# Kernel optimization log

Measured on AMD Instinct MI355X. Metric: run time of the kernel, lower is better.

## Reference

```python
import jax, jax.numpy as jnp
import numpy as np

NUM_HEADS = 128
QK_NOPE = 128
QK_ROPE = 64
V_HEAD = 128
Q_HEAD_DIM = 192
SOFTMAX_SCALE = 1.0 / np.sqrt(192.0)


def _rope_interleave(x, cos, sin):
    # x: [b,h,s,d]; reorder interleaved pairs to half-split layout then rotate
    b, h, s, d = x.shape
    x = x.reshape(b, h, s, d // 2, 2).swapaxes(3, 4).reshape(b, h, s, d)
    x1, x2 = x[..., : d // 2], x[..., d // 2:]
    rot = jnp.concatenate([-x2, x1], axis=-1)
    return x * cos + rot * sin


def setup_inputs() -> dict:
    key = jax.random.key(0)
    ks = jax.random.split(key, 8)
    bsz, q_len = 16, 1
    q_lora, kv_lora = 1536, 512
    cache_cap = 4096
    start_pos = 2048
    s = 0.05
    q_normed_dn = jax.random.normal(ks[0], (bsz, q_len, q_lora), jnp.float32) * s
    compressed_kv = jax.random.normal(ks[1], (bsz, q_len, kv_lora), jnp.float32) * s
    k_pe = jax.random.normal(ks[2], (bsz, 1, q_len, QK_ROPE), jnp.float32) * s
    position_ids = jnp.full((bsz, q_len), start_pos, dtype=jnp.int64)
    ckv_cache = jax.random.normal(ks[3], (bsz, cache_cap, kv_lora), jnp.float32) * s
    k_pe_cache = jax.random.normal(ks[4], (bsz, cache_cap, QK_ROPE), jnp.float32) * s
    # rope caches over full positions
    pos = jnp.arange(cache_cap, dtype=jnp.float32)
    inv = 1.0 / (10000.0 ** (jnp.arange(0, QK_ROPE, 2, dtype=jnp.float32) / QK_ROPE))
    freqs = pos[:, None] * inv[None, :]
    emb = jnp.concatenate([freqs, freqs], axis=-1)
    sin_cache = jnp.sin(emb)
    cos_cache = jnp.cos(emb)
    wkv_b = jax.random.normal(ks[5], (NUM_HEADS, QK_NOPE + V_HEAD, kv_lora), jnp.float32) * s
    wq_b = jax.random.normal(ks[6], (NUM_HEADS * Q_HEAD_DIM, q_lora), jnp.float32) * s
    return {
        "q_normed_dn": q_normed_dn,
        "compressed_kv": compressed_kv,
        "k_pe": k_pe,
        "position_ids": position_ids,
        "start_pos": start_pos,
        "ckv_cache": ckv_cache,
        "k_pe_cache": k_pe_cache,
        "sin_cache": sin_cache,
        "cos_cache": cos_cache,
        "wkv_b": wkv_b,
        "wq_b": wq_b,
    }


def reference(q_normed_dn, compressed_kv, k_pe, position_ids, start_pos,
              ckv_cache, k_pe_cache, sin_cache, cos_cache, wkv_b, wq_b):
    bsz, q_len, q_lora = q_normed_dn.shape
    kv_lora = compressed_kv.shape[-1]

    # split absorbed query projection
    wq_b_t = wq_b.T.reshape(q_lora, NUM_HEADS, Q_HEAD_DIM)  # [l,h,192]
    q_nope = jnp.einsum('bsl,lhd->bhsd', q_normed_dn, wq_b_t[:, :, :QK_NOPE])
    q_pe = jnp.einsum('bsl,lhd->bhsd', q_normed_dn, wq_b_t[:, :, QK_NOPE:])

    # matrix absorption: q_nope projected into latent space via w_ukv
    w_ukv = wkv_b[:, :QK_NOPE]                         # [h,128,c]
    q_nope = jnp.einsum('bshd,hdc->bshc', q_nope.swapaxes(1, 2), w_ukv)  # [b,s,h,c]

    # RoPE on q_pe and k_pe using gathered cos/sin at position_ids
    cos = cos_cache[position_ids][:, None]   # [b,1,s,d]
    sin = sin_cache[position_ids][:, None]
    q_pe = _rope_interleave(q_pe, cos, sin)            # [b,h,s,64]
    k_pe = _rope_interleave(k_pe, cos, sin)            # [b,1,s,64]
    q_pe = q_pe.swapaxes(1, 2)                         # [b,s,h,64]
    k_pe = k_pe[:, 0]                                  # [b,s,64]

    # append new tokens to caches at start_pos (q_len new tokens)
    ckv_cache = jax.lax.dynamic_update_slice(ckv_cache, compressed_kv, (0, start_pos, 0))
    k_pe_cache = jax.lax.dynamic_update_slice(k_pe_cache, k_pe, (0, start_pos, 0))
    kv_len = start_pos + q_len
    ckv = ckv_cache[:, :kv_len]                        # [b,n,c]
    kpe = k_pe_cache[:, :kv_len]                       # [b,n,64]

    # MLA decode attention in latent space (q_len==1, causal trivially satisfied)
    # scores = q_nope . ckv + q_pe . kpe
    scores = (jnp.einsum('bshc,bnc->bhsn', q_nope, ckv) +
              jnp.einsum('bshd,bnd->bhsn', q_pe, kpe)) * SOFTMAX_SCALE
    probs = jax.nn.softmax(scores, axis=-1)
    o = jnp.einsum('bhsn,bnc->bshc', probs, ckv)       # [b,s,h,c]
    o = o.reshape(bsz * q_len, NUM_HEADS, kv_lora)

    # project latent output to v_head_dim via tail of wkv_b
    attn_output = jnp.einsum('bhc,hdc->bhd', o, wkv_b[:, -V_HEAD:])
    return attn_output
```

## Files before the change

kernel.cpp:

```cpp
#include <hip/hip_runtime.h>
#include <hip/hip_bf16.h>
#include <math.h>

typedef __attribute__((ext_vector_type(8))) short short8x;
typedef __attribute__((ext_vector_type(4))) float f32x4;
typedef __attribute__((ext_vector_type(4))) unsigned short u16x4;
typedef __attribute__((ext_vector_type(8))) unsigned short u16x8;

#define NSPLIT 16
#define NTILE 66
#define KVROWS (NTILE * 32)

__device__ __forceinline__ unsigned short f2bf(float x) {
  unsigned int u = __float_as_uint(x);
  u += 0x7fffu + ((u >> 16) & 1u);
  return (unsigned short)(u >> 16);
}
__device__ __forceinline__ float bf2f(unsigned short u) {
  return __uint_as_float(((unsigned int)u) << 16);
}
__device__ __forceinline__ u16x4 cvt4(float4 v) {
  u16x4 r;
  r[0] = f2bf(v.x); r[1] = f2bf(v.y); r[2] = f2bf(v.z); r[3] = f2bf(v.w);
  return r;
}
__device__ __forceinline__ void gload_lds16(const void* g, void* l) {
  __builtin_amdgcn_global_load_lds(
      (const __attribute__((address_space(1))) unsigned int*)g,
      (__attribute__((address_space(3))) unsigned int*)l, 16, 0, 0);
}

__global__ __launch_bounds__(256) void kP_prep(
    const float* __restrict__ ckvc, const float* __restrict__ kpec,
    const float* __restrict__ ckvn, const float* __restrict__ kpein,
    const float* __restrict__ cosc, const float* __restrict__ sinc,
    const int* __restrict__ sposp, int cap,
    unsigned short* __restrict__ kvbf,
    const float* __restrict__ x,
    unsigned short* __restrict__ xh, unsigned short* __restrict__ xl) {
  const int bx = blockIdx.x;
  const int tid = threadIdx.x;
  const int spos = sposp[0];

  if (bx < 2376) {
#pragma unroll
    for (int i = 0; i < 8; ++i) {
      const int u = bx * 2048 + i * 256 + tid;
      const int b = u / 304128;
      const int r = u - b * 304128;
      const int n = r / 144;
      const int c4 = (r - n * 144) * 4;
      float4 v = make_float4(0.f, 0.f, 0.f, 0.f);
      if (n < spos) {
        if (c4 < 512) v = *(const float4*)(ckvc + ((size_t)b * cap + n) * 512 + c4);
        else          v = *(const float4*)(kpec + ((size_t)b * cap + n) * 64 + (c4 - 512));
      } else if (n == spos) {
        if (c4 < 512) v = *(const float4*)(ckvn + (size_t)b * 512 + c4);
        else {
          const int d = c4 - 512;
          const float* kp = kpein + b * 64;
          float o[4];
          if (d < 32) {
#pragma unroll
            for (int k = 0; k < 4; ++k) {
              int j = d + k;
              o[k] = kp[2 * j] * cosc[spos * 64 + j] - kp[2 * j + 1] * sinc[spos * 64 + j];
            }
          } else {
#pragma unroll
            for (int k = 0; k < 4; ++k) {
              int j = d - 32 + k;
              o[k] = kp[2 * j + 1] * cosc[spos * 64 + j] + kp[2 * j] * sinc[spos * 64 + j];
            }
          }
          v = make_float4(o[0], o[1], o[2], o[3]);
        }
      }
      *(u16x4*)(kvbf + (size_t)u * 4) = cvt4(v);
    }
  } else {
#pragma unroll
    for (int i = 0; i < 24; ++i) {
      const int u = i * 256 + tid;
      const float4 v = *(const float4*)(x + u * 4);
      const float vf[4] = {v.x, v.y, v.z, v.w};
      u16x4 h, l;
#pragma unroll
      for (int k = 0; k < 4; ++k) {
        const unsigned int uu = __float_as_uint(vf[k]);
        const unsigned int hb = uu & 0xffff0000u;
        h[k] = (unsigned short)(hb >> 16);
        l[k] = f2bf(vf[k] - __uint_as_float(hb));
      }
      *(u16x4*)(xh + u * 4) = h;
      *(u16x4*)(xl + u * 4) = l;
    }
  }
}

__global__ __launch_bounds__(256) void kVT(
    const unsigned short* __restrict__ kvbf, unsigned short* __restrict__ vT) {
  __shared__ __align__(16) unsigned short tile_sh[32 * 576];
  const int v_ = blockIdx.x;
  const int b = v_ / NTILE;
  const int tile = v_ - b * NTILE;
  const int tid = threadIdx.x;
  const int wid = tid >> 6;
  const unsigned short* src = kvbf + ((size_t)b * KVROWS + tile * 32) * 576;

#pragma unroll
  for (int i = 0; i < 9; ++i) {
    const int ch = i * 256 + tid;
    const int row = ch / 72, cc = ch - row * 72;
    gload_lds16(src + row * 576 + ((cc ^ (row & 7)) * 8),
                &tile_sh[(i * 256 + wid * 64) * 8]);
  }
  __syncthreads();

  unsigned short* vdst = vT + ((size_t)b * NTILE + tile) * 18432;
#pragma unroll
  for (int r = 0; r < 9; ++r) {
    const int c = r * 64 + (tid >> 2);
    const int q = tid & 3;
    const int c8 = c >> 3, c7 = c & 7;
    u16x8 w;
#pragma unroll
    for (int j = 0; j < 8; ++j)
      w[j] = tile_sh[(q * 8 + j) * 576 + ((c8 ^ j) << 3) + c7];
    *(u16x8*)(vdst + c * 32 + q * 8) = w;
  }
}

__global__ __launch_bounds__(256) void k1q(
    const float* __restrict__ wq,
    const unsigned short* __restrict__ xh, const unsigned short* __restrict__ xl,
    float* __restrict__ qfull) {
  const int tid = threadIdx.x;
  const int lane = tid & 63, wid = tid >> 6;
  const int l15 = lane & 15, lg = lane >> 4;
  const int rowb = blockIdx.x * 64 + wid * 16;
  const float* wrow = wq + (size_t)(rowb + l15) * 1536 + lg * 8;
  const unsigned short* xhp = xh + l15 * 1536 + lg * 8;
  const unsigned short* xlp = xl + l15 * 1536 + lg * 8;

  f32x4 acc = (f32x4){0.f, 0.f, 0.f, 0.f};
#pragma unroll 8
  for (int kc = 0; kc < 48; ++kc) {
    const float4 wA = *(const float4*)(wrow + kc * 32);
    const float4 wB = *(const float4*)(wrow + kc * 32 + 4);
    const short8x bh = *(const short8x*)(xhp + kc * 32);
    const short8x bl = *(const short8x*)(xlp + kc * 32);
    const float wf[8] = {wA.x, wA.y, wA.z, wA.w, wB.x, wB.y, wB.z, wB.w};
    short8x ah, al;
#pragma unroll
    for (int e = 0; e < 8; ++e) {
      const unsigned int uu = __float_as_uint(wf[e]);
      const unsigned int hb = uu & 0xffff0000u;
      ah[e] = (short)(hb >> 16);
      al[e] = (short)f2bf(wf[e] - __uint_as_float(hb));
    }
    acc = __builtin_amdgcn_mfma_f32_16x16x32_bf16(ah, bh, acc, 0, 0, 0);
    acc = __builtin_amdgcn_mfma_f32_16x16x32_bf16(ah, bl, acc, 0, 0, 0);
    acc = __builtin_amdgcn_mfma_f32_16x16x32_bf16(al, bh, acc, 0, 0, 0);
  }
#pragma unroll
  for (int r = 0; r < 4; ++r)
    qfull[(size_t)l15 * 24576 + rowb + lg * 4 + r] = acc[r];
}

__global__ __launch_bounds__(256) void kB_q(
    const float* __restrict__ qfull, const float* __restrict__ wkv,
    const float* __restrict__ cosc, const float* __restrict__ sinc,
    const int* __restrict__ sposp, unsigned short* __restrict__ qcat) {
  __shared__ float qs[16 * 128];
  const int bx = blockIdx.x;
  const int tid = threadIdx.x;
  if (bx < 256) {
    const int h = bx & 127;
    const int half = bx >> 7;
    for (int u = tid; u < 2048; u += 256) {
      int bb = u >> 7, d = u & 127;
      qs[u] = qfull[bb * 24576 + h * 192 + d];
    }
    __syncthreads();
    const int c = half * 256 + tid;
    float acc[16];
#pragma unroll
    for (int bb = 0; bb < 16; ++bb) acc[bb] = 0.f;
    const float* wbase = wkv + (size_t)h * 256 * 512;
    for (int d = 0; d < 128; ++d) {
      const float w = wbase[d * 512 + c];
#pragma unroll
      for (int bb = 0; bb < 16; ++bb) acc[bb] += qs[bb * 128 + d] * w;
    }
#pragma unroll
    for (int bb = 0; bb < 16; ++bb)
      qcat[(size_t)(bb * 128 + h) * 576 + c] = f2bf(acc[bb]);
  } else {
    const int b = bx - 256;
    const int pos = sposp[0];
#pragma unroll
    for (int i = 0; i < 16; ++i) {
      int idx = tid + i * 256;
      int h = idx >> 5, j = idx & 31;
      const float cj = cosc[pos * 64 + j];
      const float sj = sinc[pos * 64 + j];
      const float* src = qfull + b * 24576 + h * 192 + 128;
      float x0 = src[2 * j], x1 = src[2 * j + 1];
      unsigned short* dst = qcat + (size_t)(b * 128 + h) * 576 + 512;
      dst[j] = f2bf(x0 * cj - x1 * sj);
      dst[j + 32] = f2bf(x1 * cj + x0 * sj);
    }
  }
}

__global__ __launch_bounds__(512, 2) void k4_attn(
    const unsigned short* __restrict__ kvbf, const unsigned short* __restrict__ vT,
    const unsigned short* __restrict__ qcat, const int* __restrict__ sposp,
    unsigned short* __restrict__ opart, float* __restrict__ mlp) {
  __shared__ __align__(16) unsigned short kv_sh[2][32 * 576];
  __shared__ __align__(16) unsigned short vt_sh[2][512 * 32];
  __shared__ __align__(16) unsigned short p_sh[8 * 640];

  const int tid = threadIdx.x;
  const int split = blockIdx.x, b = blockIdx.y;
  const int kvlen = sposp[0] + 1;
  const int lane = tid & 63, wid = tid >> 6;
  const int l15 = lane & 15, lg = lane >> 4;

  const unsigned short* kvb = kvbf + (size_t)b * KVROWS * 576;
  const unsigned short* vtb = vT + (size_t)b * NTILE * 18432;

  auto STAGE = [&](int pb, int tt) {
    const unsigned short* ksrc = kvb + (size_t)tt * 32 * 576;
    for (int j = wid; j < 36; j += 8) {
      int u = j * 64 + lane;
      int row = u / 72, cc = u - row * 72;
      gload_lds16(ksrc + row * 576 + ((cc ^ (row & 7)) * 8), &kv_sh[pb][j * 512]);
    }
    const unsigned short* vsrc = vtb + (size_t)tt * 18432;
    for (int j = wid; j < 32; j += 8)
      gload_lds16(vsrc + j * 512 + lane * 8, &vt_sh[pb][j * 512]);
  };

  STAGE(0, split);

  const int hrow = b * 128 + wid * 16 + l15;
  const unsigned short* qrow = qcat + (size_t)hrow * 576;
  short8x qf[18];
#pragma unroll
  for (int s = 0; s < 18; ++s)
    qf[s] = *(const short8x*)(qrow + s * 32 + lg * 8);

  f32x4 acc[32];
#pragma unroll
  for (int i = 0; i < 32; ++i) acc[i] = (f32x4){0.f, 0.f, 0.f, 0.f};
  float mold[4] = {-1e30f, -1e30f, -1e30f, -1e30f};
  float lsum[4] = {0.f, 0.f, 0.f, 0.f};
  const float C2 = (1.0f / sqrtf(192.0f)) * 1.4426950408889634f;

  int pb = 0;
  for (int tt = split; tt * 32 < kvlen; tt += NSPLIT, pb ^= 1) {
    __syncthreads();
    if ((tt + NSPLIT) * 32 < kvlen) STAGE(pb ^ 1, tt + NSPLIT);
    const int n0 = tt * 32;

    f32x4 D0 = (f32x4){0.f, 0.f, 0.f, 0.f};
    f32x4 D1 = (f32x4){0.f, 0.f, 0.f, 0.f};
#pragma unroll
    for (int s = 0; s < 18; ++s) {
      const int c8 = (s * 4 + lg) ^ (l15 & 7);
      short8x fb0 = *(const short8x*)&kv_sh[pb][l15 * 576 + c8 * 8];
      short8x fb1 = *(const short8x*)&kv_sh[pb][(16 + l15) * 576 + c8 * 8];
      D0 = __builtin_amdgcn_mfma_f32_16x16x32_bf16(qf[s], fb0, D0, 0, 0, 0);
      D1 = __builtin_amdgcn_mfma_f32_16x16x32_bf16(qf[s], fb1, D1, 0, 0, 0);
    }

    const bool v0 = (n0 + l15) < kvlen;
    const bool v1 = (n0 + 16 + l15) < kvlen;
    float alpha[4];
#pragma unroll
    for (int r = 0; r < 4; ++r) {
      const float t0 = v0 ? D0[r] * C2 : -1e30f;
      const float t1 = v1 ? D1[r] * C2 : -1e30f;
      float mx = fmaxf(t0, t1);
      mx = fmaxf(mx, __shfl_xor(mx, 1, 64));
      mx = fmaxf(mx, __shfl_xor(mx, 2, 64));
      mx = fmaxf(mx, __shfl_xor(mx, 4, 64));
      mx = fmaxf(mx, __shfl_xor(mx, 8, 64));
      const float mn = fmaxf(mold[r], mx);
      alpha[r] = exp2f(mold[r] - mn);
      const float p0 = v0 ? exp2f(t0 - mn) : 0.f;
      const float p1 = v1 ? exp2f(t1 - mn) : 0.f;
      float rs = p0 + p1;
      rs += __shfl_xor(rs, 1, 64);
      rs += __shfl_xor(rs, 2, 64);
      rs += __shfl_xor(rs, 4, 64);
      rs += __shfl_xor(rs, 8, 64);
      lsum[r] = lsum[r] * alpha[r] + rs;
      mold[r] = mn;
      p_sh[wid * 640 + (lg * 4 + r) * 40 + l15] = f2bf(p0);
      p_sh[wid * 640 + (lg * 4 + r) * 40 + 16 + l15] = f2bf(p1);
    }
    const f32x4 av = {alpha[0], alpha[1], alpha[2], alpha[3]};
#pragma unroll
    for (int cg = 0; cg < 32; ++cg) acc[cg] *= av;

    const short8x pa = *(const short8x*)&p_sh[wid * 640 + l15 * 40 + lg * 8];
#pragma unroll
    for (int cg = 0; cg < 32; ++cg) {
      short8x bv = *(const short8x*)&vt_sh[pb][cg * 512 + l15 * 32 + lg * 8];
      acc[cg] = __builtin_amdgcn_mfma_f32_16x16x32_bf16(pa, bv, acc[cg], 0, 0, 0);
    }
  }

  const int hbm_ = b * 128 + wid * 16 + lg * 4;
  if (l15 == 0) {
#pragma unroll
    for (int r = 0; r < 4; ++r) {
      mlp[(size_t)(hbm_ + r) * (2 * NSPLIT) + split * 2] = mold[r];
      mlp[(size_t)(hbm_ + r) * (2 * NSPLIT) + split * 2 + 1] = lsum[r];
    }
  }

  __syncthreads();
  unsigned short* ep = &kv_sh[0][0] + wid * 8192;
#pragma unroll
  for (int cg = 0; cg < 32; ++cg)
#pragma unroll
    for (int r = 0; r < 4; ++r)
      ep[(lg * 4 + r) * 512 + cg * 16 + l15] = f2bf(acc[cg][r]);
#pragma unroll
  for (int r16 = 0; r16 < 16; ++r16) {
    const int bh = b * 128 + wid * 16 + r16;
    const size_t ob = ((size_t)bh * NSPLIT + split) * 512;
#pragma unroll
    for (int i = 0; i < 2; ++i)
      *(u16x4*)&opart[ob + i * 256 + lane * 4] =
          *(const u16x4*)&ep[r16 * 512 + i * 256 + lane * 4];
  }
}

__global__ __launch_bounds__(512) void kC_out(
    const unsigned short* __restrict__ opart, const float* __restrict__ mlp,
    const float* __restrict__ wkv, float* __restrict__ out) {
  __shared__ float os[16 * 512];
  __shared__ float wsc[16 * 16];
  __shared__ float lsc[16];
  const int h = blockIdx.x;
  const int tid = threadIdx.x;

  if (tid < 16) {
    const int b = tid;
    const float* m = mlp + (size_t)(b * 128 + h) * (2 * NSPLIT);
    float mi[NSPLIT], li[NSPLIT], M = -1e30f;
#pragma unroll
    for (int i = 0; i < NSPLIT; ++i) {
      mi[i] = m[i * 2];
      li[i] = m[i * 2 + 1];
      M = fmaxf(M, mi[i]);
    }
    float Ls = 0.f;
#pragma unroll
    for (int i = 0; i < NSPLIT; ++i) {
      const float w = exp2f(mi[i] - M);
      Ls += li[i] * w;
      wsc[b * NSPLIT + i] = w;
    }
    lsc[b] = Ls;
  }
  __syncthreads();

  for (int u = tid; u < 8192; u += 512) {
    const int b = u >> 9, c = u & 511;
    const unsigned short* op = opart + (size_t)(b * 128 + h) * NSPLIT * 512 + c;
    float o = 0.f;
#pragma unroll
    for (int i = 0; i < NSPLIT; ++i) o += wsc[b * NSPLIT + i] * bf2f(op[i * 512]);
    os[u] = o / lsc[b];
  }
  __syncthreads();

  const int d = tid >> 2, cq = tid & 3;
  const float* wrow = wkv + ((size_t)(h * 256 + 128 + d)) * 512;
  float acc[16];
#pragma unroll
  for (int bb = 0; bb < 16; ++bb) acc[bb] = 0.f;
  for (int i = 0; i < 32; ++i) {
    const int c = cq * 4 + i * 16;
    const float4 w4 = *(const float4*)&wrow[c];
#pragma unroll
    for (int bb = 0; bb < 16; ++bb) {
      const float4 o4 = *(const float4*)&os[bb * 512 + c];
      acc[bb] += w4.x * o4.x + w4.y * o4.y + w4.z * o4.z + w4.w * o4.w;
    }
  }
#pragma unroll
  for (int bb = 0; bb < 16; ++bb) {
    float v = acc[bb];
    v += __shfl_xor(v, 1, 64);
    v += __shfl_xor(v, 2, 64);
    if (cq == 0) out[(size_t)(bb * 128 + h) * 128 + d] = v;
  }
}

extern "C" void kernel_launch(void* const* d_in, const int* in_sizes, int n_in,
                              void* d_out, int out_size, void* d_ws, size_t ws_size,
                              hipStream_t stream) {
  const float* x = (const float*)d_in[0];
  const float* ckvn = (const float*)d_in[1];
  const float* kpein = (const float*)d_in[2];
  const int* sposp = (const int*)d_in[4];
  const float* ckvc = (const float*)d_in[5];
  const float* kpec = (const float*)d_in[6];
  const float* sinc = (const float*)d_in[7];
  const float* cosc = (const float*)d_in[8];
  const float* wkv = (const float*)d_in[9];
  const float* wq = (const float*)d_in[10];
  float* out = (float*)d_out;

  const int cap = in_sizes[5] / (16 * 512);

  float* ws = (float*)d_ws;
  float* qfull = ws;
  float* mlp = ws + 393216;
  unsigned short* qcat = (unsigned short*)(ws + 458752);
  unsigned short* xh   = (unsigned short*)(ws + 1048576);
  unsigned short* xl   = (unsigned short*)(ws + 1060864);
  unsigned short* kvbf = (unsigned short*)(ws + 1073152);
  unsigned short* vT   = (unsigned short*)(ws + 10805248);
  unsigned short* opart = (unsigned short*)(ws + 20537344);

  kP_prep<<<dim3(2377), 256, 0, stream>>>(ckvc, kpec, ckvn, kpein, cosc, sinc,
                                          sposp, cap, kvbf, x, xh, xl);
  kVT<<<dim3(1056), 256, 0, stream>>>(kvbf, vT);
  k1q<<<dim3(384), 256, 0, stream>>>(wq, xh, xl, qfull);
  kB_q<<<dim3(272), 256, 0, stream>>>(qfull, wkv, cosc, sinc, sposp, qcat);
  k4_attn<<<dim3(NSPLIT, 16), 512, 0, stream>>>(kvbf, vT, qcat, sposp, opart, mlp);
  kC_out<<<dim3(128), 512, 0, stream>>>(opart, mlp, wkv, out);
}
```

Measured before the change: 184.9 us.

## Fuse KV bf16 conversion with V transpose and split x in GEMM

Merges the KV-cache bf16 conversion kernel and the separate V-transpose kernel into one per-tile kernel. It loads fp32 rows into LDS with a swizzle and writes both the row-major bf16 K copy and the transposed V copy, so the bf16 intermediate is no longer re-read. The hi/lo bf16 split of the query input moves into the q-projection GEMM, removing the xh/xl buffers and one launch. The cost is that fp32 is read twice: once from global memory for K and once via LDS for V. The LDS tile also doubles to 72KB, which may lower occupancy.

```diff
diff --git a/kernel.cpp b/kernel.cpp
--- a/kernel.cpp
+++ b/kernel.cpp
@@ -30,26 +30,75 @@
       (__attribute__((address_space(3))) unsigned int*)l, 16, 0, 0);
 }
 
-__global__ __launch_bounds__(256) void kP_prep(
+__global__ __launch_bounds__(256) void kPV(
     const float* __restrict__ ckvc, const float* __restrict__ kpec,
     const float* __restrict__ ckvn, const float* __restrict__ kpein,
     const float* __restrict__ cosc, const float* __restrict__ sinc,
     const int* __restrict__ sposp, int cap,
-    unsigned short* __restrict__ kvbf,
-    const float* __restrict__ x,
-    unsigned short* __restrict__ xh, unsigned short* __restrict__ xl) {
-  const int bx = blockIdx.x;
+    unsigned short* __restrict__ kvbf, unsigned short* __restrict__ vT) {
+  __shared__ __align__(16) float tile_sh[32 * 576];
+  const int v_ = blockIdx.x;
+  const int b = v_ / NTILE;
+  const int tile = v_ - b * NTILE;
+  const int n0 = tile * 32;
   const int tid = threadIdx.x;
+  const int wid = tid >> 6;
   const int spos = sposp[0];
 
-  if (bx < 2376) {
-#pragma unroll
-    for (int i = 0; i < 8; ++i) {
-      const int u = bx * 2048 + i * 256 + tid;
-      const int b = u / 304128;
-      const int r = u - b * 304128;
-      const int n = r / 144;
-      const int c4 = (r - n * 144) * 4;
+  unsigned short* kdst = kvbf + ((size_t)b * KVROWS + n0) * 576;
+  unsigned short* vdst = vT + ((size_t)b * NTILE + tile) * 18432;
+
+  if (n0 + 31 < spos) {
+    const float* cbase = ckvc + ((size_t)b * cap + n0) * 512;
+    const float* pbase = kpec + ((size_t)b * cap + n0) * 64;
+#pragma unroll
+    for (int i = 0; i < 18; ++i) {
+      const int ch = i * 256 + tid;
+      const int row = ch / 144, cc = ch - row * 144;
+      const int gc = cc ^ (row & 7);
+      const float* src = (gc < 128) ? cbase + (size_t)row * 512 + gc * 4
+                                    : pbase + (size_t)row * 64 + (gc - 128) * 4;
+      gload_lds16(src, &tile_sh[(i * 256 + wid * 64) * 4]);
+    }
+#pragma unroll
+    for (int i = 0; i < 9; ++i) {
+      const int oc = i * 256 + tid;
+      const int row = oc / 72, p = oc - row * 72;
+      const int c0 = p * 8;
+      float4 a, c2;
+      if (c0 < 512) {
+        a  = *(const float4*)(cbase + (size_t)row * 512 + c0);
+        c2 = *(const float4*)(cbase + (size_t)row * 512 + c0 + 4);
+      } else {
+        a  = *(const float4*)(pbase + (size_t)row * 64 + (c0 - 512));
+        c2 = *(const float4*)(pbase + (size_t)row * 64 + (c0 - 512) + 4);
+      }
+      const u16x4 wa = cvt4(a), wb = cvt4(c2);
+      u16x8 w;
+#pragma unroll
+      for (int k = 0; k < 4; ++k) { w[k] = wa[k]; w[4 + k] = wb[k]; }
+      *(u16x8*)(kdst + row * 576 + c0) = w;
+    }
+    __syncthreads();
+#pragma unroll
+    for (int r = 0; r < 9; ++r) {
+      const int c = r * 64 + (tid >> 2);
+      const int q = tid & 3;
+      const int gc = c >> 2, c3 = c & 3;
+      u16x8 w;
+#pragma unroll
+      for (int j = 0; j < 8; ++j) {
+        const int n = q * 8 + j;
+        w[j] = f2bf(tile_sh[n * 576 + ((gc ^ j) << 2) + c3]);
+      }
+      *(u16x8*)(vdst + c * 32 + q * 8) = w;
+    }
+  } else if (n0 <= spos) {
+#pragma unroll
+    for (int i = 0; i < 18; ++i) {
+      const int u = i * 256 + tid;
+      const int row = u / 144, c4 = (u - row * 144) * 4;
+      const int n = n0 + row;
       float4 v = make_float4(0.f, 0.f, 0.f, 0.f);
       if (n < spos) {
         if (c4 < 512) v = *(const float4*)(ckvc + ((size_t)b * cap + n) * 512 + c4);
@@ -76,88 +125,77 @@
           v = make_float4(o[0], o[1], o[2], o[3]);
         }
       }
-      *(u16x4*)(kvbf + (size_t)u * 4) = cvt4(v);
+      *(u16x4*)(kdst + row * 576 + c4) = cvt4(v);
+    }
+#pragma unroll
+    for (int i = 0; i < 18; ++i) {
+      const int o = i * 256 + tid;
+      const int c = o >> 3;
+      const int n4 = (o & 7) * 4;
+      u16x4 w;
+#pragma unroll
+      for (int k = 0; k < 4; ++k) {
+        const int n = n0 + n4 + k;
+        float x = 0.f;
+        if (n < spos) {
+          x = (c < 512) ? ckvc[((size_t)b * cap + n) * 512 + c]
+                        : kpec[((size_t)b * cap + n) * 64 + (c - 512)];
+        } else if (n == spos) {
+          if (c < 512) x = ckvn[(size_t)b * 512 + c];
+          else {
+            const int d = c - 512;
+            const float* kp = kpein + b * 64;
+            const int j = (d < 32) ? d : d - 32;
+            const float cj = cosc[spos * 64 + j], sj = sinc[spos * 64 + j];
+            x = (d < 32) ? kp[2 * j] * cj - kp[2 * j + 1] * sj
+                         : kp[2 * j + 1] * cj + kp[2 * j] * sj;
+          }
+        }
+        w[k] = f2bf(x);
+      }
+      *(u16x4*)(vdst + c * 32 + n4) = w;
     }
   } else {
-#pragma unroll
-    for (int i = 0; i < 24; ++i) {
-      const int u = i * 256 + tid;
-      const float4 v = *(const float4*)(x + u * 4);
-      const float vf[4] = {v.x, v.y, v.z, v.w};
-      u16x4 h, l;
-#pragma unroll
-      for (int k = 0; k < 4; ++k) {
-        const unsigned int uu = __float_as_uint(vf[k]);
-        const unsigned int hb = uu & 0xffff0000u;
-        h[k] = (unsigned short)(hb >> 16);
-        l[k] = f2bf(vf[k] - __uint_as_float(hb));
-      }
-      *(u16x4*)(xh + u * 4) = h;
-      *(u16x4*)(xl + u * 4) = l;
-    }
-  }
-}
-
-__global__ __launch_bounds__(256) void kVT(
-    const unsigned short* __restrict__ kvbf, unsigned short* __restrict__ vT) {
-  __shared__ __align__(16) unsigned short tile_sh[32 * 576];
-  const int v_ = blockIdx.x;
-  const int b = v_ / NTILE;
-  const int tile = v_ - b * NTILE;
-  const int tid = threadIdx.x;
-  const int wid = tid >> 6;
-  const unsigned short* src = kvbf + ((size_t)b * KVROWS + tile * 32) * 576;
-
-#pragma unroll
-  for (int i = 0; i < 9; ++i) {
-    const int ch = i * 256 + tid;
-    const int row = ch / 72, cc = ch - row * 72;
-    gload_lds16(src + row * 576 + ((cc ^ (row & 7)) * 8),
-                &tile_sh[(i * 256 + wid * 64) * 8]);
-  }
-  __syncthreads();
-
-  unsigned short* vdst = vT + ((size_t)b * NTILE + tile) * 18432;
-#pragma unroll
-  for (int r = 0; r < 9; ++r) {
-    const int c = r * 64 + (tid >> 2);
-    const int q = tid & 3;
-    const int c8 = c >> 3, c7 = c & 7;
-    u16x8 w;
-#pragma unroll
-    for (int j = 0; j < 8; ++j)
-      w[j] = tile_sh[(q * 8 + j) * 576 + ((c8 ^ j) << 3) + c7];
-    *(u16x8*)(vdst + c * 32 + q * 8) = w;
+    const u16x8 z = {0, 0, 0, 0, 0, 0, 0, 0};
+#pragma unroll
+    for (int i = 0; i < 9; ++i) {
+      const int oc = i * 256 + tid;
+      *(u16x8*)(kdst + oc * 8) = z;
+      *(u16x8*)(vdst + oc * 8) = z;
+    }
   }
 }
 
 __global__ __launch_bounds__(256) void k1q(
-    const float* __restrict__ wq,
-    const unsigned short* __restrict__ xh, const unsigned short* __restrict__ xl,
+    const float* __restrict__ wq, const float* __restrict__ x,
     float* __restrict__ qfull) {
   const int tid = threadIdx.x;
   const int lane = tid & 63, wid = tid >> 6;
   const int l15 = lane & 15, lg = lane >> 4;
   const int rowb = blockIdx.x * 64 + wid * 16;
   const float* wrow = wq + (size_t)(rowb + l15) * 1536 + lg * 8;
-  const unsigned short* xhp = xh + l15 * 1536 + lg * 8;
-  const unsigned short* xlp = xl + l15 * 1536 + lg * 8;
+  const float* xrow = x + l15 * 1536 + lg * 8;
 
   f32x4 acc = (f32x4){0.f, 0.f, 0.f, 0.f};
 #pragma unroll 8
   for (int kc = 0; kc < 48; ++kc) {
     const float4 wA = *(const float4*)(wrow + kc * 32);
     const float4 wB = *(const float4*)(wrow + kc * 32 + 4);
-    const short8x bh = *(const short8x*)(xhp + kc * 32);
-    const short8x bl = *(const short8x*)(xlp + kc * 32);
+    const float4 xA = *(const float4*)(xrow + kc * 32);
+    const float4 xB = *(const float4*)(xrow + kc * 32 + 4);
     const float wf[8] = {wA.x, wA.y, wA.z, wA.w, wB.x, wB.y, wB.z, wB.w};
-    short8x ah, al;
+    const float xf[8] = {xA.x, xA.y, xA.z, xA.w, xB.x, xB.y, xB.z, xB.w};
+    short8x ah, al, bh, bl;
 #pragma unroll
     for (int e = 0; e < 8; ++e) {
-      const unsigned int uu = __float_as_uint(wf[e]);
-      const unsigned int hb = uu & 0xffff0000u;
+      unsigned int uu = __float_as_uint(wf[e]);
+      unsigned int hb = uu & 0xffff0000u;
       ah[e] = (short)(hb >> 16);
       al[e] = (short)f2bf(wf[e] - __uint_as_float(hb));
+      uu = __float_as_uint(xf[e]);
+      hb = uu & 0xffff0000u;
+      bh[e] = (short)(hb >> 16);
+      bl[e] = (short)f2bf(xf[e] - __uint_as_float(hb));
     }
     acc = __builtin_amdgcn_mfma_f32_16x16x32_bf16(ah, bh, acc, 0, 0, 0);
     acc = __builtin_amdgcn_mfma_f32_16x16x32_bf16(ah, bl, acc, 0, 0, 0);
@@ -425,16 +463,13 @@
   float* qfull = ws;
   float* mlp = ws + 393216;
   unsigned short* qcat = (unsigned short*)(ws + 458752);
-  unsigned short* xh   = (unsigned short*)(ws + 1048576);
-  unsigned short* xl   = (unsigned short*)(ws + 1060864);
-  unsigned short* kvbf = (unsigned short*)(ws + 1073152);
-  unsigned short* vT   = (unsigned short*)(ws + 10805248);
-  unsigned short* opart = (unsigned short*)(ws + 20537344);
-
-  kP_prep<<<dim3(2377), 256, 0, stream>>>(ckvc, kpec, ckvn, kpein, cosc, sinc,
-                                          sposp, cap, kvbf, x, xh, xl);
-  kVT<<<dim3(1056), 256, 0, stream>>>(kvbf, vT);
-  k1q<<<dim3(384), 256, 0, stream>>>(wq, xh, xl, qfull);
+  unsigned short* kvbf = (unsigned short*)(ws + 1048576);
+  unsigned short* vT   = (unsigned short*)(ws + 10780672);
+  unsigned short* opart = (unsigned short*)(ws + 20512768);
+
+  kPV<<<dim3(NTILE * 16), 256, 0, stream>>>(ckvc, kpec, ckvn, kpein, cosc, sinc,
+                                            sposp, cap, kvbf, vT);
+  k1q<<<dim3(384), 256, 0, stream>>>(wq, x, qfull);
   kB_q<<<dim3(272), 256, 0, stream>>>(qfull, wkv, cosc, sinc, sposp, qcat);
   k4_attn<<<dim3(NSPLIT, 16), 512, 0, stream>>>(kvbf, vT, qcat, sposp, opart, mlp);
   kC_out<<<dim3(128), 512, 0, stream>>>(opart, mlp, wkv, out);
```

Measured after the change: 202.4 us. 9.4% more time.

## Merge prep, q-projection and V-transpose kernels into fewer launches; swizzle V LDS

Applied to the files above, without the earlier changes.

Fuses the fp32 q projection (now splitting x into hi/lo bf16 inline, so the separate xh/xl pass goes away) into the KV bf16 conversion kernel as extra blocks. The V-transpose kernel is folded into the q-absorption kernel as extra blocks, cutting six launches to four and letting independent work share the GPU. The attention kernel also applies an XOR swizzle to the V tile layout in LDS to reduce bank conflicts on the P·V reads. The cost is repeated hi/lo conversion of x in every q block and a larger shared allocation for the merged kernel.

```diff
diff --git a/kernel.cpp b/kernel.cpp
--- a/kernel.cpp
+++ b/kernel.cpp
@@ -30,22 +30,58 @@
       (__attribute__((address_space(3))) unsigned int*)l, 16, 0, 0);
 }
 
-__global__ __launch_bounds__(256) void kP_prep(
+__global__ __launch_bounds__(256) void kA(
     const float* __restrict__ ckvc, const float* __restrict__ kpec,
     const float* __restrict__ ckvn, const float* __restrict__ kpein,
     const float* __restrict__ cosc, const float* __restrict__ sinc,
     const int* __restrict__ sposp, int cap,
     unsigned short* __restrict__ kvbf,
-    const float* __restrict__ x,
-    unsigned short* __restrict__ xh, unsigned short* __restrict__ xl) {
+    const float* __restrict__ wq, const float* __restrict__ x,
+    float* __restrict__ qfull) {
   const int bx = blockIdx.x;
   const int tid = threadIdx.x;
-  const int spos = sposp[0];
-
-  if (bx < 2376) {
+
+  if (bx < 384) {
+    const int lane = tid & 63, wid = tid >> 6;
+    const int l15 = lane & 15, lg = lane >> 4;
+    const int rowb = bx * 64 + wid * 16;
+    const float* wrow = wq + (size_t)(rowb + l15) * 1536 + lg * 8;
+    const float* xrow = x + l15 * 1536 + lg * 8;
+
+    f32x4 acc = (f32x4){0.f, 0.f, 0.f, 0.f};
+#pragma unroll 8
+    for (int kc = 0; kc < 48; ++kc) {
+      const float4 wA = *(const float4*)(wrow + kc * 32);
+      const float4 wB = *(const float4*)(wrow + kc * 32 + 4);
+      const float4 xA = *(const float4*)(xrow + kc * 32);
+      const float4 xB = *(const float4*)(xrow + kc * 32 + 4);
+      const float wf[8] = {wA.x, wA.y, wA.z, wA.w, wB.x, wB.y, wB.z, wB.w};
+      const float xf[8] = {xA.x, xA.y, xA.z, xA.w, xB.x, xB.y, xB.z, xB.w};
+      short8x ah, al, bh, bl;
+#pragma unroll
+      for (int e = 0; e < 8; ++e) {
+        unsigned int uu = __float_as_uint(wf[e]);
+        unsigned int hb = uu & 0xffff0000u;
+        ah[e] = (short)(hb >> 16);
+        al[e] = (short)f2bf(wf[e] - __uint_as_float(hb));
+        uu = __float_as_uint(xf[e]);
+        hb = uu & 0xffff0000u;
+        bh[e] = (short)(hb >> 16);
+        bl[e] = (short)f2bf(xf[e] - __uint_as_float(hb));
+      }
+      acc = __builtin_amdgcn_mfma_f32_16x16x32_bf16(ah, bh, acc, 0, 0, 0);
+      acc = __builtin_amdgcn_mfma_f32_16x16x32_bf16(ah, bl, acc, 0, 0, 0);
+      acc = __builtin_amdgcn_mfma_f32_16x16x32_bf16(al, bh, acc, 0, 0, 0);
+    }
+#pragma unroll
+    for (int r = 0; r < 4; ++r)
+      qfull[(size_t)l15 * 24576 + rowb + lg * 4 + r] = acc[r];
+  } else {
+    const int bxx = bx - 384;
+    const int spos = sposp[0];
 #pragma unroll
     for (int i = 0; i < 8; ++i) {
-      const int u = bx * 2048 + i * 256 + tid;
+      const int u = bxx * 2048 + i * 256 + tid;
       const int b = u / 304128;
       const int r = u - b * 304128;
       const int n = r / 144;
@@ -78,104 +114,20 @@
       }
       *(u16x4*)(kvbf + (size_t)u * 4) = cvt4(v);
     }
-  } else {
-#pragma unroll
-    for (int i = 0; i < 24; ++i) {
-      const int u = i * 256 + tid;
-      const float4 v = *(const float4*)(x + u * 4);
-      const float vf[4] = {v.x, v.y, v.z, v.w};
-      u16x4 h, l;
-#pragma unroll
-      for (int k = 0; k < 4; ++k) {
-        const unsigned int uu = __float_as_uint(vf[k]);
-        const unsigned int hb = uu & 0xffff0000u;
-        h[k] = (unsigned short)(hb >> 16);
-        l[k] = f2bf(vf[k] - __uint_as_float(hb));
-      }
-      *(u16x4*)(xh + u * 4) = h;
-      *(u16x4*)(xl + u * 4) = l;
-    }
-  }
-}
-
-__global__ __launch_bounds__(256) void kVT(
-    const unsigned short* __restrict__ kvbf, unsigned short* __restrict__ vT) {
-  __shared__ __align__(16) unsigned short tile_sh[32 * 576];
-  const int v_ = blockIdx.x;
-  const int b = v_ / NTILE;
-  const int tile = v_ - b * NTILE;
-  const int tid = threadIdx.x;
-  const int wid = tid >> 6;
-  const unsigned short* src = kvbf + ((size_t)b * KVROWS + tile * 32) * 576;
-
-#pragma unroll
-  for (int i = 0; i < 9; ++i) {
-    const int ch = i * 256 + tid;
-    const int row = ch / 72, cc = ch - row * 72;
-    gload_lds16(src + row * 576 + ((cc ^ (row & 7)) * 8),
-                &tile_sh[(i * 256 + wid * 64) * 8]);
-  }
-  __syncthreads();
-
-  unsigned short* vdst = vT + ((size_t)b * NTILE + tile) * 18432;
-#pragma unroll
-  for (int r = 0; r < 9; ++r) {
-    const int c = r * 64 + (tid >> 2);
-    const int q = tid & 3;
-    const int c8 = c >> 3, c7 = c & 7;
-    u16x8 w;
-#pragma unroll
-    for (int j = 0; j < 8; ++j)
-      w[j] = tile_sh[(q * 8 + j) * 576 + ((c8 ^ j) << 3) + c7];
-    *(u16x8*)(vdst + c * 32 + q * 8) = w;
-  }
-}
-
-__global__ __launch_bounds__(256) void k1q(
-    const float* __restrict__ wq,
-    const unsigned short* __restrict__ xh, const unsigned short* __restrict__ xl,
-    float* __restrict__ qfull) {
-  const int tid = threadIdx.x;
-  const int lane = tid & 63, wid = tid >> 6;
-  const int l15 = lane & 15, lg = lane >> 4;
-  const int rowb = blockIdx.x * 64 + wid * 16;
-  const float* wrow = wq + (size_t)(rowb + l15) * 1536 + lg * 8;
-  const unsigned short* xhp = xh + l15 * 1536 + lg * 8;
-  const unsigned short* xlp = xl + l15 * 1536 + lg * 8;
-
-  f32x4 acc = (f32x4){0.f, 0.f, 0.f, 0.f};
-#pragma unroll 8
-  for (int kc = 0; kc < 48; ++kc) {
-    const float4 wA = *(const float4*)(wrow + kc * 32);
-    const float4 wB = *(const float4*)(wrow + kc * 32 + 4);
-    const short8x bh = *(const short8x*)(xhp + kc * 32);
-    const short8x bl = *(const short8x*)(xlp + kc * 32);
-    const float wf[8] = {wA.x, wA.y, wA.z, wA.w, wB.x, wB.y, wB.z, wB.w};
-    short8x ah, al;
-#pragma unroll
-    for (int e = 0; e < 8; ++e) {
-      const unsigned int uu = __float_as_uint(wf[e]);
-      const unsigned int hb = uu & 0xffff0000u;
-      ah[e] = (short)(hb >> 16);
-      al[e] = (short)f2bf(wf[e] - __uint_as_float(hb));
-    }
-    acc = __builtin_amdgcn_mfma_f32_16x16x32_bf16(ah, bh, acc, 0, 0, 0);
-    acc = __builtin_amdgcn_mfma_f32_16x16x32_bf16(ah, bl, acc, 0, 0, 0);
-    acc = __builtin_amdgcn_mfma_f32_16x16x32_bf16(al, bh, acc, 0, 0, 0);
-  }
-#pragma unroll
-  for (int r = 0; r < 4; ++r)
-    qfull[(size_t)l15 * 24576 + rowb + lg * 4 + r] = acc[r];
-}
-
-__global__ __launch_bounds__(256) void kB_q(
+  }
+}
+
+__global__ __launch_bounds__(256) void kB2(
     const float* __restrict__ qfull, const float* __restrict__ wkv,
     const float* __restrict__ cosc, const float* __restrict__ sinc,
-    const int* __restrict__ sposp, unsigned short* __restrict__ qcat) {
-  __shared__ float qs[16 * 128];
+    const int* __restrict__ sposp, unsigned short* __restrict__ qcat,
+    const unsigned short* __restrict__ kvbf, unsigned short* __restrict__ vT) {
+  __shared__ __align__(16) unsigned char shbuf[36864];
   const int bx = blockIdx.x;
   const int tid = threadIdx.x;
+
   if (bx < 256) {
+    float* qs = (float*)shbuf;
     const int h = bx & 127;
     const int half = bx >> 7;
     for (int u = tid; u < 2048; u += 256) {
@@ -196,7 +148,7 @@
 #pragma unroll
     for (int bb = 0; bb < 16; ++bb)
       qcat[(size_t)(bb * 128 + h) * 576 + c] = f2bf(acc[bb]);
-  } else {
+  } else if (bx < 272) {
     const int b = bx - 256;
     const int pos = sposp[0];
 #pragma unroll
@@ -211,6 +163,33 @@
       dst[j] = f2bf(x0 * cj - x1 * sj);
       dst[j + 32] = f2bf(x1 * cj + x0 * sj);
     }
+  } else {
+    unsigned short* tile_sh = (unsigned short*)shbuf;
+    const int v_ = bx - 272;
+    const int b = v_ / NTILE;
+    const int tile = v_ - b * NTILE;
+    const int wid = tid >> 6;
+    const unsigned short* src = kvbf + ((size_t)b * KVROWS + tile * 32) * 576;
+#pragma unroll
+    for (int i = 0; i < 9; ++i) {
+      const int ch = i * 256 + tid;
+      const int row = ch / 72, cc = ch - row * 72;
+      gload_lds16(src + row * 576 + ((cc ^ (row & 7)) * 8),
+                  &tile_sh[(i * 256 + wid * 64) * 8]);
+    }
+    __syncthreads();
+    unsigned short* vdst = vT + ((size_t)b * NTILE + tile) * 18432;
+#pragma unroll
+    for (int r = 0; r < 9; ++r) {
+      const int c = r * 64 + (tid >> 2);
+      const int q = tid & 3;
+      const int c8 = c >> 3, c7 = c & 7;
+      u16x8 w;
+#pragma unroll
+      for (int j = 0; j < 8; ++j)
+        w[j] = tile_sh[(q * 8 + j) * 576 + ((c8 ^ j) << 3) + c7];
+      *(u16x8*)(vdst + c * 32 + q * 8) = w;
+    }
   }
 }
 
@@ -231,6 +210,9 @@
   const unsigned short* kvb = kvbf + (size_t)b * KVROWS * 576;
   const unsigned short* vtb = vT + (size_t)b * NTILE * 18432;
 
+  const int vro = lane >> 2, vq = lane & 3;
+  const int vgq = vq ^ ((vro >> 1) & 3);
+
   auto STAGE = [&](int pb, int tt) {
     const unsigned short* ksrc = kvb + (size_t)tt * 32 * 576;
     for (int j = wid; j < 36; j += 8) {
@@ -240,7 +222,7 @@
     }
     const unsigned short* vsrc = vtb + (size_t)tt * 18432;
     for (int j = wid; j < 32; j += 8)
-      gload_lds16(vsrc + j * 512 + lane * 8, &vt_sh[pb][j * 512]);
+      gload_lds16(vsrc + j * 512 + vro * 32 + vgq * 8, &vt_sh[pb][j * 512]);
   };
 
   STAGE(0, split);
@@ -258,6 +240,8 @@
   float mold[4] = {-1e30f, -1e30f, -1e30f, -1e30f};
   float lsum[4] = {0.f, 0.f, 0.f, 0.f};
   const float C2 = (1.0f / sqrtf(192.0f)) * 1.4426950408889634f;
+
+  const int vrd = ((lg ^ ((l15 >> 1) & 3)) << 3);
 
   int pb = 0;
   for (int tt = split; tt * 32 < kvlen; tt += NSPLIT, pb ^= 1) {
@@ -309,7 +293,7 @@
     const short8x pa = *(const short8x*)&p_sh[wid * 640 + l15 * 40 + lg * 8];
 #pragma unroll
     for (int cg = 0; cg < 32; ++cg) {
-      short8x bv = *(const short8x*)&vt_sh[pb][cg * 512 + l15 * 32 + lg * 8];
+      short8x bv = *(const short8x*)&vt_sh[pb][cg * 512 + l15 * 32 + vrd];
       acc[cg] = __builtin_amdgcn_mfma_f32_16x16x32_bf16(pa, bv, acc[cg], 0, 0, 0);
     }
   }
@@ -425,17 +409,14 @@
   float* qfull = ws;
   float* mlp = ws + 393216;
   unsigned short* qcat = (unsigned short*)(ws + 458752);
-  unsigned short* xh   = (unsigned short*)(ws + 1048576);
-  unsigned short* xl   = (unsigned short*)(ws + 1060864);
-  unsigned short* kvbf = (unsigned short*)(ws + 1073152);
-  unsigned short* vT   = (unsigned short*)(ws + 10805248);
-  unsigned short* opart = (unsigned short*)(ws + 20537344);
-
-  kP_prep<<<dim3(2377), 256, 0, stream>>>(ckvc, kpec, ckvn, kpein, cosc, sinc,
-                                          sposp, cap, kvbf, x, xh, xl);
-  kVT<<<dim3(1056), 256, 0, stream>>>(kvbf, vT);
-  k1q<<<dim3(384), 256, 0, stream>>>(wq, xh, xl, qfull);
-  kB_q<<<dim3(272), 256, 0, stream>>>(qfull, wkv, cosc, sinc, sposp, qcat);
+  unsigned short* kvbf = (unsigned short*)(ws + 1048576);
+  unsigned short* vT   = (unsigned short*)(ws + 10780672);
+  unsigned short* opart = (unsigned short*)(ws + 20512768);
+
+  kA<<<dim3(384 + 2376), 256, 0, stream>>>(ckvc, kpec, ckvn, kpein, cosc, sinc,
+                                           sposp, cap, kvbf, wq, x, qfull);
+  kB2<<<dim3(272 + NTILE * 16), 256, 0, stream>>>(qfull, wkv, cosc, sinc, sposp,
+                                                  qcat, kvbf, vT);
   k4_attn<<<dim3(NSPLIT, 16), 512, 0, stream>>>(kvbf, vT, qcat, sposp, opart, mlp);
   kC_out<<<dim3(128), 512, 0, stream>>>(opart, mlp, wkv, out);
 }
```

Result: faster. 175.8 us (-4.9%).
